# Kernel optimization log

Hardware: AMD Instinct MI355X
Metric: run time of the kernel (lower is better)

The kernel has to match this reference:

```python
import jax, jax.numpy as jnp
import numpy as np

IMG = 256      # image size implied by 8x8 grid * scale 32
THRE = 0.5
DIS = 4        # img_dislocate_size
B = 64


def _shift_map(s, size, dis):
    # Pixel-level coordinate map for the dislocated half: cell r starts at
    # max(r*s - dis, 0) (the torch while-loop clamps negative coords to 0).
    p = jnp.arange(size)
    base = jnp.maximum((p // s) * s - dis, 0)
    return base + p % s


def _cell_norm(x, g, s):
    # Per-cell (crop) min/max normalization, matching the per-crop
    # (t - min) / (max - min + 1e-5) in HeatMaptoImg.
    b = x.shape[0]
    v = x.reshape(b, 1, g, s, g, s)
    mn = v.min(axis=(3, 5), keepdims=True)
    mx = v.max(axis=(3, 5), keepdims=True)
    return ((v - mn) / (mx - mn + 1e-5)).reshape(b, 1, g * s, g * s)


def setup_inputs() -> dict:
    key = jax.random.key(0)
    ks = jax.random.split(key, 7)
    B2 = 2 * B
    return {
        "img": jax.random.uniform(ks[0], (B, 1, IMG, IMG), jnp.float32),
        "heat8": jax.random.uniform(ks[1], (B2, 1, 8, 8), jnp.float32),
        "heat16": jax.random.uniform(ks[2], (B2, 1, 16, 16), jnp.float32),
        "heat32": jax.random.uniform(ks[3], (B2, 1, 32, 32), jnp.float32),
        "seg8": jax.random.uniform(ks[4], (B2, 1, IMG, IMG), jnp.float32),
        "seg16": jax.random.uniform(ks[5], (B2, 1, IMG, IMG), jnp.float32),
        "seg32": jax.random.uniform(ks[6], (B2, 1, IMG, IMG), jnp.float32),
    }


def reference(img, heat8, heat16, heat32, seg8, seg16, seg32):
    Bv = img.shape[0]
    label = jnp.zeros((Bv, 1, IMG, IMG), img.dtype)
    cnt = jnp.zeros_like(label)
    crops = {}
    # fine grid (scale 8) processed first, matching the reversed loop order
    for heat, seg, g in ((heat32, seg32, 32), (heat16, seg16, 16), (heat8, seg8, 8)):
        s = IMG // g                      # crop / cell size for this scale
        mask = (heat > THRE).astype(img.dtype)          # (2B,1,g,g)
        mask_pix = jnp.repeat(jnp.repeat(mask, s, axis=2), s, axis=3)  # (2B,1,256,256)
        Y = _shift_map(s, IMG, DIS)
        # dislocated half crops come from the shifted image region
        img_d = img[:, :, Y[:, None], Y[None, :]]       # (B,1,256,256)
        both = jnp.concatenate([img, img_d], axis=0)    # (2B,1,256,256)
        crops[g] = _cell_norm(both, g, s) * mask_pix
        # UnitLabels: scatter-add per-crop labels + counts, then average
        ca = mask_pix[:Bv]
        label = label + ca * seg[:Bv]
        cnt = cnt + ca
        cd = mask_pix[Bv:]
        label = label.at[:, :, Y[:, None], Y[None, :]].add(cd * seg[Bv:])
        cnt = cnt.at[:, :, Y[:, None], Y[None, :]].add(cd)
    label = label / (cnt + 1e-10)
    return (crops[32], crops[16], crops[8], label)
```

## Files before the change

kernel.cpp:

```cpp
#include <hip/hip_runtime.h>

#define IMG   256
#define IMG2  65536
#define NB    64
#define NB2   128

#define WS_A8   0
#define WS_B8   65536
#define WS_A16  131072
#define WS_B16  147456
#define WS_A32  163840
#define WS_B32  167936
#define WS_BLK  172032

__global__ __launch_bounds__(256) void blk_kernel(
    const float* __restrict__ img, float2* __restrict__ ws) {
    const int wid  = blockIdx.x * 4 + (threadIdx.x >> 6);
    const int lane = threadIdx.x & 63;
    const int b    = wid >> 6;
    const int r4   = wid & 63;
    const float* __restrict__ p =
        img + (size_t)b * IMG2 + (r4 * 4) * IMG + lane * 4;
    const float4 q0 = *(const float4*)(p);
    const float4 q1 = *(const float4*)(p + IMG);
    const float4 q2 = *(const float4*)(p + 2 * IMG);
    const float4 q3 = *(const float4*)(p + 3 * IMG);
    const float mn01 = fminf(fminf(fminf(q0.x, q0.y), fminf(q0.z, q0.w)),
                             fminf(fminf(q1.x, q1.y), fminf(q1.z, q1.w)));
    const float mn23 = fminf(fminf(fminf(q2.x, q2.y), fminf(q2.z, q2.w)),
                             fminf(fminf(q3.x, q3.y), fminf(q3.z, q3.w)));
    const float mx01 = fmaxf(fmaxf(fmaxf(q0.x, q0.y), fmaxf(q0.z, q0.w)),
                             fmaxf(fmaxf(q1.x, q1.y), fmaxf(q1.z, q1.w)));
    const float mx23 = fmaxf(fmaxf(fmaxf(q2.x, q2.y), fmaxf(q2.z, q2.w)),
                             fmaxf(fmaxf(q3.x, q3.y), fmaxf(q3.z, q3.w)));
    ws[WS_BLK + (b << 12) + (r4 << 6) + lane] =
        make_float2(fminf(mn01, mn23), fmaxf(mx01, mx23));
}

template <int SH>
__device__ __forceinline__ float2 combine_blk(
    const float2* __restrict__ blk, int b, int p0, int q0) {
    float mn = 3.4e38f, mx = -3.4e38f;
    for (int i = 0; i < SH; ++i) {
#pragma unroll
        for (int j = 0; j < SH; ++j) {
            const float2 v = blk[(b << 12) + ((p0 + i) << 6) + (q0 + j)];
            mn = fminf(mn, v.x);
            mx = fmaxf(mx, v.y);
        }
    }
    return make_float2(mn, mx);
}

__device__ __forceinline__ float2 finish(float2 c, float h) {
    return make_float2(c.x, (h > 0.5f ? 1.0f : 0.0f) / (c.y - c.x + 1e-5f));
}

__global__ __launch_bounds__(256) void cells_kernel(
    const float* __restrict__ heat8,
    const float* __restrict__ heat16,
    const float* __restrict__ heat32,
    float2* __restrict__ ws) {
    const float2* __restrict__ blk = ws + WS_BLK;
    const int t = blockIdx.x * 256 + threadIdx.x;
    if (t < 131072) {
        const int idx = t & 65535;
        const int half = t >> 16;
        const int b = idx >> 10, ci = (idx >> 5) & 31, cj = idx & 31;
        const int p0 = half ? max(2 * ci - 1, 0) : 2 * ci;
        const int q0 = half ? max(2 * cj - 1, 0) : 2 * cj;
        const float2 c = combine_blk<2>(blk, b, p0, q0);
        const float h = heat32[(size_t)(b + half * NB) * 1024 + ci * 32 + cj];
        ws[(half ? WS_B8 : WS_A8) + idx] = finish(c, h);
    } else if (t < 163840) {
        const int tt = t - 131072;
        const int idx = tt & 16383;
        const int half = tt >> 14;
        const int b = idx >> 8, ci = (idx >> 4) & 15, cj = idx & 15;
        const int p0 = half ? max(4 * ci - 1, 0) : 4 * ci;
        const int q0 = half ? max(4 * cj - 1, 0) : 4 * cj;
        const float2 c = combine_blk<4>(blk, b, p0, q0);
        const float h = heat16[(size_t)(b + half * NB) * 256 + ci * 16 + cj];
        ws[(half ? WS_B16 : WS_A16) + idx] = finish(c, h);
    } else {
        const int tt = t - 163840;
        const int idx = tt & 4095;
        const int half = tt >> 12;
        const int b = idx >> 6, ci = (idx >> 3) & 7, cj = idx & 7;
        const int p0 = half ? max(8 * ci - 1, 0) : 8 * ci;
        const int q0 = half ? max(8 * cj - 1, 0) : 8 * cj;
        const float2 c = combine_blk<8>(blk, b, p0, q0);
        const float h = heat8[(size_t)(b + half * NB) * 64 + ci * 8 + cj];
        ws[(half ? WS_B32 : WS_A32) + idx] = finish(c, h);
    }
}

__global__ __launch_bounds__(256) void crops_stream_kernel(
    const float* __restrict__ img,
    const float2* __restrict__ ws,
    float* __restrict__ out) {
    const int tid = blockIdx.x * 256 + threadIdx.x;
    float* __restrict__ c32 = out;
    float* __restrict__ c16 = out + (size_t)NB2 * IMG2;
    float* __restrict__ c8  = out + (size_t)2 * NB2 * IMG2;

#pragma unroll
    for (int ph = 0; ph < 6; ++ph) {
#pragma unroll
        for (int k = 0; k < 2; ++k) {
            const int i  = tid + k * 524288;
            const int b  = i >> 14;
            const int u  = (i >> 6) & 255;
            const int v0 = (i & 63) << 2;
            const float* __restrict__ ip = img + (size_t)b * IMG2;

            int srow, scol;
            float2 st;
            float* optr;
            switch (ph) {
            case 0:
                srow = u; scol = v0;
                st = ws[WS_A8 + (b << 10) + ((u >> 3) << 5) + (v0 >> 3)];
                optr = c32 + (size_t)b * IMG2;
                break;
            case 1:
                srow = ((u >> 3) ? (u & ~7) - 4 : 0) + (u & 7);
                scol = (v0 < 8) ? v0 : v0 - 4;
                st = ws[WS_B8 + (b << 10) + ((u >> 3) << 5) + (v0 >> 3)];
                optr = c32 + (size_t)(b + NB) * IMG2;
                break;
            case 2:
                srow = u; scol = v0;
                st = ws[WS_A16 + (b << 8) + ((u >> 4) << 4) + (v0 >> 4)];
                optr = c16 + (size_t)b * IMG2;
                break;
            case 3:
                srow = ((u >> 4) ? (u & ~15) - 4 : 0) + (u & 15);
                scol = (v0 < 16) ? v0 : v0 - 4;
                st = ws[WS_B16 + (b << 8) + ((u >> 4) << 4) + (v0 >> 4)];
                optr = c16 + (size_t)(b + NB) * IMG2;
                break;
            case 4:
                srow = u; scol = v0;
                st = ws[WS_A32 + (b << 6) + ((u >> 5) << 3) + (v0 >> 5)];
                optr = c8 + (size_t)b * IMG2;
                break;
            default:
                srow = ((u >> 5) ? (u & ~31) - 4 : 0) + (u & 31);
                scol = (v0 < 32) ? v0 : v0 - 4;
                st = ws[WS_B32 + (b << 6) + ((u >> 5) << 3) + (v0 >> 5)];
                optr = c8 + (size_t)(b + NB) * IMG2;
                break;
            }
            const float4 q = *(const float4*)(ip + srow * IMG + scol);
            float4 o;
            o.x = (q.x - st.x) * st.y; o.y = (q.y - st.x) * st.y;
            o.z = (q.z - st.x) * st.y; o.w = (q.w - st.x) * st.y;
            *(float4*)(optr + u * IMG + v0) = o;
        }
    }
}

__device__ __forceinline__ void label_rows(
    const float* __restrict__ heat8,
    const float* __restrict__ heat16,
    const float* __restrict__ heat32,
    const float* __restrict__ seg8,
    const float* __restrict__ seg16,
    const float* __restrict__ seg32,
    float* __restrict__ out,
    int b, int u0) {
    const int wave = threadIdx.x >> 6;
    const int lane = threadIdx.x & 63;
    const int u    = u0 + wave;
    const int v0   = lane << 2;
    const int vs   = min(v0 + 4, 252);

    float nu[4] = {0.f, 0.f, 0.f, 0.f};
    float de[4] = {0.f, 0.f, 0.f, 0.f};

    if (u0 >= 32 && u0 <= 248) {
        const int i1 = u + 4;
#define SCALE_F(heat, seg, g, l, s)                                           \
        {                                                                     \
            const float* __restrict__ h1 = heat + b * (g * g);                \
            const float* __restrict__ h2 = heat + (NB + b) * (g * g);         \
            const float* __restrict__ r1 = seg + (size_t)b * IMG2 + u * IMG;  \
            const float* __restrict__ r2 =                                    \
                seg + (size_t)(NB + b) * IMG2 + i1 * IMG;                     \
            const float4 sd  = *(const float4*)(r1 + v0);                     \
            const float4 sg0 = *(const float4*)(r2 + v0);                     \
            const float4 sg1 = *(const float4*)(r2 + vs);                     \
            const float hd  = h1[(u >> l) * g + (v0 >> l)];                   \
            const float hg0 = h2[(i1 >> l) * g + (v0 >> l)];                  \
            const float hg1 = h2[(i1 >> l) * g + (vs >> l)];                  \
            const float md = (hd > 0.5f) ? 1.0f : 0.0f;                       \
            const float g0 = (hg0 > 0.5f) ? 1.0f : 0.0f;                      \
            const float g1 = (hg1 > 0.5f) ? 1.0f : 0.0f;                      \
            _Pragma("unroll")                                                 \
            for (int c = 0; c < 4; ++c) {                                     \
                const int v = v0 + c;                                         \
                const float m0 = (v < (s)) ? g0 : 0.0f;                       \
                const float m1 = (v >= (s) - 4 && v <= 251) ? g1 : 0.0f;      \
                float x = ((const float*)&sd)[c] * md;                        \
                x = fmaf(m0, ((const float*)&sg0)[c], x);                     \
                x = fmaf(m1, ((const float*)&sg1)[c], x);                     \
                nu[c] += x;                                                   \
                de[c] += md + m0 + m1;                                        \
            }                                                                 \
        }
        SCALE_F(heat32, seg32, 32, 3, 8)
        SCALE_F(heat16, seg16, 16, 4, 16)
        SCALE_F(heat8,  seg8,  8,  5, 32)
#undef SCALE_F
    } else {
        const int i0  = u;
        const int i1c = min(u + 4, 255);
#define SCALE_G(heat, seg, g, l, s)                                           \
        {                                                                     \
            const float* __restrict__ h1 = heat + b * (g * g);                \
            const float* __restrict__ h2 = heat + (NB + b) * (g * g);         \
            const float* __restrict__ r1 = seg + (size_t)b * IMG2 + u * IMG;  \
            const float* __restrict__ ra =                                    \
                seg + (size_t)(NB + b) * IMG2 + i0 * IMG;                     \
            const float* __restrict__ rb =                                    \
                seg + (size_t)(NB + b) * IMG2 + i1c * IMG;                    \
            const float4 sd  = *(const float4*)(r1 + v0);                     \
            const float4 a0q = *(const float4*)(ra + v0);                     \
            const float4 a1q = *(const float4*)(ra + vs);                     \
            const float4 b0q = *(const float4*)(rb + v0);                     \
            const float4 b1q = *(const float4*)(rb + vs);                     \
            const float hd  = h1[(u >> l) * g + (v0 >> l)];                   \
            const float hA0 = h2[(i0 >> l) * g + (v0 >> l)];                  \
            const float hA1 = h2[(i0 >> l) * g + (vs >> l)];                  \
            const float hB0 = h2[(i1c >> l) * g + (v0 >> l)];                 \
            const float hB1 = h2[(i1c >> l) * g + (vs >> l)];                 \
            const float miA = (u < (s)) ? 1.0f : 0.0f;                        \
            const float miB = (u >= (s) - 4 && u <= 251) ? 1.0f : 0.0f;       \
            const float md  = (hd > 0.5f) ? 1.0f : 0.0f;                      \
            const float gA0 = miA * ((hA0 > 0.5f) ? 1.0f : 0.0f);             \
            const float gA1 = miA * ((hA1 > 0.5f) ? 1.0f : 0.0f);             \
            const float gB0 = miB * ((hB0 > 0.5f) ? 1.0f : 0.0f);             \
            const float gB1 = miB * ((hB1 > 0.5f) ? 1.0f : 0.0f);             \
            _Pragma("unroll")                                                 \
            for (int c = 0; c < 4; ++c) {                                     \
                const int v = v0 + c;                                         \
                const float mj0 = (v < (s)) ? 1.0f : 0.0f;                    \
                const float mj1 = (v >= (s) - 4 && v <= 251) ? 1.0f : 0.0f;   \
                const float w00 = gA0 * mj0, w01 = gA1 * mj1;                 \
                const float w10 = gB0 * mj0, w11 = gB1 * mj1;                 \
                float x = ((const float*)&sd)[c] * md;                        \
                x = fmaf(w00, ((const float*)&a0q)[c], x);                    \
                x = fmaf(w01, ((const float*)&a1q)[c], x);                    \
                x = fmaf(w10, ((const float*)&b0q)[c], x);                    \
                x = fmaf(w11, ((const float*)&b1q)[c], x);                    \
                nu[c] += x;                                                   \
                de[c] += md + w00 + w01 + w10 + w11;                          \
            }                                                                 \
        }
        SCALE_G(heat32, seg32, 32, 3, 8)
        SCALE_G(heat16, seg16, 16, 4, 16)
        SCALE_G(heat8,  seg8,  8,  5, 32)
#undef SCALE_G
    }

    float4 o;
    o.x = nu[0] / (de[0] + 1e-10f);
    o.y = nu[1] / (de[1] + 1e-10f);
    o.z = nu[2] / (de[2] + 1e-10f);
    o.w = nu[3] / (de[3] + 1e-10f);
    *(float4*)(out + (size_t)b * IMG2 + u * IMG + v0) = o;
}

__global__ __launch_bounds__(256) void label_kernel(
    const float* __restrict__ heat8,
    const float* __restrict__ heat16,
    const float* __restrict__ heat32,
    const float* __restrict__ seg8,
    const float* __restrict__ seg16,
    const float* __restrict__ seg32,
    float* __restrict__ out) {
    float* label = out + (size_t)3 * NB2 * IMG2;
    const int t  = blockIdx.x;
    label_rows(heat8, heat16, heat32, seg8, seg16, seg32, label,
               t >> 6, (t & 63) << 2);
}

extern "C" void kernel_launch(void* const* d_in, const int* in_sizes, int n_in,
                              void* d_out, int out_size, void* d_ws, size_t ws_size,
                              hipStream_t stream) {
    const float* img    = (const float*)d_in[0];
    const float* heat8  = (const float*)d_in[1];
    const float* heat16 = (const float*)d_in[2];
    const float* heat32 = (const float*)d_in[3];
    const float* seg8   = (const float*)d_in[4];
    const float* seg16  = (const float*)d_in[5];
    const float* seg32  = (const float*)d_in[6];
    float2* ws = (float2*)d_ws;

    blk_kernel<<<dim3(1024), 256, 0, stream>>>(img, ws);
    cells_kernel<<<dim3(672), 256, 0, stream>>>(heat8, heat16, heat32, ws);
    crops_stream_kernel<<<dim3(2048), 256, 0, stream>>>(
        img, (const float2*)ws, (float*)d_out);
    label_kernel<<<dim3(4096), 256, 0, stream>>>(
        heat8, heat16, heat32, seg8, seg16, seg32, (float*)d_out);
}
```

Measured before the change: 228.2 us.

## Replace crops streaming kernel with grid-barrier phased load-then-store kernel

The crops kernel becomes a 512-block persistent kernel. Each thread first loads all image and statistics values for its 8 positions across the 6 outputs and holds the normalized results in registers. It then waits on a global atomic barrier, with a clock timeout, before all blocks write their outputs, so reads and writes are separated into distinct phases instead of interleaved. The label kernel is also moved ahead of the stats kernels. This risks register spills from the 48 float4 values per thread, deadlock or timeout if not all 512 blocks are co-resident, and spin overhead.

Result: slower. 252.2 us (+10.5%).

```diff
diff --git a/kernel.cpp b/kernel.cpp
--- a/kernel.cpp
+++ b/kernel.cpp
@@ -12,9 +12,12 @@
 #define WS_A32  163840
 #define WS_B32  167936
 #define WS_BLK  172032
+#define WS_BAR_BYTES  3473408
 
 __global__ __launch_bounds__(256) void blk_kernel(
-    const float* __restrict__ img, float2* __restrict__ ws) {
+    const float* __restrict__ img, float2* __restrict__ ws,
+    unsigned* __restrict__ bar) {
+    if (blockIdx.x == 0 && threadIdx.x == 0) bar[0] = 0u;
     const int wid  = blockIdx.x * 4 + (threadIdx.x >> 6);
     const int lane = threadIdx.x & 63;
     const int b    = wid >> 6;
@@ -95,68 +98,79 @@
     }
 }
 
-__global__ __launch_bounds__(256) void crops_stream_kernel(
+__device__ __forceinline__ float4 nrm(float4 q, float2 st) {
+    float4 o;
+    o.x = (q.x - st.x) * st.y; o.y = (q.y - st.x) * st.y;
+    o.z = (q.z - st.x) * st.y; o.w = (q.w - st.x) * st.y;
+    return o;
+}
+
+__global__ __launch_bounds__(256, 2) void crops_coop_kernel(
     const float* __restrict__ img,
     const float2* __restrict__ ws,
-    float* __restrict__ out) {
+    float* __restrict__ out,
+    unsigned* __restrict__ bar) {
     const int tid = blockIdx.x * 256 + threadIdx.x;
+    float4 o[8][6];
+
+#pragma unroll
+    for (int j = 0; j < 8; ++j) {
+        const int pos = tid + j * 131072;
+        const int b   = pos >> 14;
+        const int u   = (pos >> 6) & 255;
+        const int v0  = (pos & 63) << 2;
+        const float* __restrict__ ip = img + (size_t)b * IMG2;
+
+        const int u8  = ((u >> 3) ? (u & ~7)  - 4 : 0) + (u & 7);
+        const int u16 = ((u >> 4) ? (u & ~15) - 4 : 0) + (u & 15);
+        const int u32 = ((u >> 5) ? (u & ~31) - 4 : 0) + (u & 31);
+        const int s8c  = (v0 < 8)  ? v0 : v0 - 4;
+        const int s16c = (v0 < 16) ? v0 : v0 - 4;
+        const int s32c = (v0 < 32) ? v0 : v0 - 4;
+
+        const float4 xa  = *(const float4*)(ip + u   * IMG + v0);
+        const float4 q8  = *(const float4*)(ip + u8  * IMG + s8c);
+        const float4 q16 = *(const float4*)(ip + u16 * IMG + s16c);
+        const float4 q32 = *(const float4*)(ip + u32 * IMG + s32c);
+
+        const float2 a8  = ws[WS_A8  + (b << 10) + ((u >> 3) << 5) + (v0 >> 3)];
+        const float2 b8  = ws[WS_B8  + (b << 10) + ((u >> 3) << 5) + (v0 >> 3)];
+        const float2 a16 = ws[WS_A16 + (b << 8)  + ((u >> 4) << 4) + (v0 >> 4)];
+        const float2 b16 = ws[WS_B16 + (b << 8)  + ((u >> 4) << 4) + (v0 >> 4)];
+        const float2 a32 = ws[WS_A32 + (b << 6)  + ((u >> 5) << 3) + (v0 >> 5)];
+        const float2 b32 = ws[WS_B32 + (b << 6)  + ((u >> 5) << 3) + (v0 >> 5)];
+
+        o[j][0] = nrm(xa,  a8);
+        o[j][1] = nrm(q8,  b8);
+        o[j][2] = nrm(xa,  a16);
+        o[j][3] = nrm(q16, b16);
+        o[j][4] = nrm(xa,  a32);
+        o[j][5] = nrm(q32, b32);
+    }
+
+    __syncthreads();
+    if (threadIdx.x == 0) {
+        atomicAdd(bar, 1u);
+        const long long t0 = clock64();
+        while (atomicAdd(bar, 0u) < 512u && (clock64() - t0) < 2000000LL) {}
+    }
+    __syncthreads();
+
     float* __restrict__ c32 = out;
     float* __restrict__ c16 = out + (size_t)NB2 * IMG2;
     float* __restrict__ c8  = out + (size_t)2 * NB2 * IMG2;
-
 #pragma unroll
-    for (int ph = 0; ph < 6; ++ph) {
+    for (int r = 0; r < 6; ++r) {
 #pragma unroll
-        for (int k = 0; k < 2; ++k) {
-            const int i  = tid + k * 524288;
-            const int b  = i >> 14;
-            const int u  = (i >> 6) & 255;
-            const int v0 = (i & 63) << 2;
-            const float* __restrict__ ip = img + (size_t)b * IMG2;
-
-            int srow, scol;
-            float2 st;
-            float* optr;
-            switch (ph) {
-            case 0:
-                srow = u; scol = v0;
-                st = ws[WS_A8 + (b << 10) + ((u >> 3) << 5) + (v0 >> 3)];
-                optr = c32 + (size_t)b * IMG2;
-                break;
-            case 1:
-                srow = ((u >> 3) ? (u & ~7) - 4 : 0) + (u & 7);
-                scol = (v0 < 8) ? v0 : v0 - 4;
-                st = ws[WS_B8 + (b << 10) + ((u >> 3) << 5) + (v0 >> 3)];
-                optr = c32 + (size_t)(b + NB) * IMG2;
-                break;
-            case 2:
-                srow = u; scol = v0;
-                st = ws[WS_A16 + (b << 8) + ((u >> 4) << 4) + (v0 >> 4)];
-                optr = c16 + (size_t)b * IMG2;
-                break;
-            case 3:
-                srow = ((u >> 4) ? (u & ~15) - 4 : 0) + (u & 15);
-                scol = (v0 < 16) ? v0 : v0 - 4;
-                st = ws[WS_B16 + (b << 8) + ((u >> 4) << 4) + (v0 >> 4)];
-                optr = c16 + (size_t)(b + NB) * IMG2;
-                break;
-            case 4:
-                srow = u; scol = v0;
-                st = ws[WS_A32 + (b << 6) + ((u >> 5) << 3) + (v0 >> 5)];
-                optr = c8 + (size_t)b * IMG2;
-                break;
-            default:
-                srow = ((u >> 5) ? (u & ~31) - 4 : 0) + (u & 31);
-                scol = (v0 < 32) ? v0 : v0 - 4;
-                st = ws[WS_B32 + (b << 6) + ((u >> 5) << 3) + (v0 >> 5)];
-                optr = c8 + (size_t)(b + NB) * IMG2;
-                break;
-            }
-            const float4 q = *(const float4*)(ip + srow * IMG + scol);
-            float4 o;
-            o.x = (q.x - st.x) * st.y; o.y = (q.y - st.x) * st.y;
-            o.z = (q.z - st.x) * st.y; o.w = (q.w - st.x) * st.y;
-            *(float4*)(optr + u * IMG + v0) = o;
+        for (int j = 0; j < 8; ++j) {
+            const int pos = tid + j * 131072;
+            const int b   = pos >> 14;
+            const int u   = (pos >> 6) & 255;
+            const int v0  = (pos & 63) << 2;
+            float* __restrict__ base =
+                (r < 2 ? c32 : (r < 4 ? c16 : c8)) +
+                (size_t)(b + ((r & 1) ? NB : 0)) * IMG2;
+            *(float4*)(base + u * IMG + v0) = o[j][r];
         }
     }
 }
@@ -296,12 +310,13 @@
     const float* seg8   = (const float*)d_in[4];
     const float* seg16  = (const float*)d_in[5];
     const float* seg32  = (const float*)d_in[6];
-    float2* ws = (float2*)d_ws;
-
-    blk_kernel<<<dim3(1024), 256, 0, stream>>>(img, ws);
-    cells_kernel<<<dim3(672), 256, 0, stream>>>(heat8, heat16, heat32, ws);
-    crops_stream_kernel<<<dim3(2048), 256, 0, stream>>>(
-        img, (const float2*)ws, (float*)d_out);
+    float2*   ws  = (float2*)d_ws;
+    unsigned* bar = (unsigned*)((char*)d_ws + WS_BAR_BYTES);
+
     label_kernel<<<dim3(4096), 256, 0, stream>>>(
         heat8, heat16, heat32, seg8, seg16, seg32, (float*)d_out);
-}
+    blk_kernel<<<dim3(1024), 256, 0, stream>>>(img, ws, bar);
+    cells_kernel<<<dim3(672), 256, 0, stream>>>(heat8, heat16, heat32, ws);
+    crops_coop_kernel<<<dim3(512), 256, 0, stream>>>(
+        img, (const float2*)ws, (float*)d_out, bar);
+}
```
